# Kernel optimization log

Hardware: AMD Instinct MI355X
Metric: run time of the kernel (lower is better)

Reference implementation:

```python
import jax, jax.numpy as jnp
import numpy as np
from jax import lax

EPS = 1e-5
B, C, H, W = 16, 256, 56, 56
HEADS, DIM_K, DIM_U, DIM_OUT = 4, 16, 4, 256
DIM_V = DIM_OUT // HEADS  # 64
R = 15


def setup_inputs() -> dict:
    key = jax.random.key(0)
    ks = jax.random.split(key, 16)
    s = 0.05
    return {
        "x": jax.random.normal(ks[0], (B, C, H, W), jnp.float32),
        "Wq": jax.random.normal(ks[1], (C, HEADS * DIM_K), jnp.float32) * s,
        "Wk": jax.random.normal(ks[2], (C, DIM_U * DIM_K), jnp.float32) * s,
        "Wv": jax.random.normal(ks[3], (C, DIM_U * DIM_V), jnp.float32) * s,
        "pos_w": jax.random.normal(ks[4], (DIM_K, DIM_U, 1, R, R), jnp.float32) * s,
        "pos_b": jax.random.normal(ks[5], (DIM_K,), jnp.float32) * s,
        "gq": jax.random.uniform(ks[6], (HEADS * DIM_K,), jnp.float32),
        "bq": jax.random.normal(ks[7], (HEADS * DIM_K,), jnp.float32) * s,
        "mq": jax.random.normal(ks[8], (HEADS * DIM_K,), jnp.float32) * s,
        "vq": jax.random.uniform(ks[9], (HEADS * DIM_K,), jnp.float32) + 0.5,
        "gv": jax.random.uniform(ks[10], (DIM_U * DIM_V,), jnp.float32),
        "bv": jax.random.normal(ks[11], (DIM_U * DIM_V,), jnp.float32) * s,
        "mv": jax.random.normal(ks[12], (DIM_U * DIM_V,), jnp.float32) * s,
        "vv": jax.random.uniform(ks[13], (DIM_U * DIM_V,), jnp.float32) + 0.5,
    }


def _bn(x, gamma, beta, mean, var):
    # inference-mode BatchNorm over channel dim (axis=1), x: [b,c,h,w]
    inv = gamma / jnp.sqrt(var + EPS)
    return x * inv[None, :, None, None] + (beta - mean * inv)[None, :, None, None]


def reference(x, Wq, Wk, Wv, pos_w, pos_b, gq, bq, mq, vq, gv, bv, mv, vv):
    b, c, hh, ww = x.shape
    n = hh * ww
    h, dk, u, dv = HEADS, DIM_K, DIM_U, DIM_V
    # 1x1 convs (channels_first) == channel matmuls
    q = jnp.einsum('bchw,cd->bdhw', x, Wq)
    k = jnp.einsum('bchw,cd->bdhw', x, Wk)
    v = jnp.einsum('bchw,cd->bdhw', x, Wv)
    q = _bn(q, gq, bq, mq, vq)
    v = _bn(v, gv, bv, mv, vv)
    # rearranges: 'b (h k) hh ww -> b h k (hh ww)', 'b (u k) hh ww -> b u k n', 'b (u v) hh ww -> b u v n'
    q = q.reshape(b, h, dk, n)
    k = k.reshape(b, u, dk, n)
    v = v.reshape(b, u, dv, n)
    k = jax.nn.softmax(k, axis=-1)  # keras Softmax default axis=-1 (positions)
    # content lambda
    Lc = jnp.einsum('bukm,buvm->bkv', k, v)
    Yc = jnp.einsum('bhkn,bkv->bnhv', q, Lc)
    # position lambda: conv3d over (v,hh,ww) with kernel (1,r,r), pad spatial only
    v5 = v.reshape(b, u, dv, hh, ww)  # [N, C=u, D=v, H, W]
    p = R // 2
    Lp = lax.conv_general_dilated(
        v5, pos_w, window_strides=(1, 1, 1),
        padding=[(0, 0), (p, p), (p, p)],
        dimension_numbers=('NCDHW', 'OIDHW', 'NCDHW'))
    Lp = Lp + pos_b[None, :, None, None, None]  # [b, k, v, hh, ww]
    Lp = Lp.reshape(b, dk, dv, n)
    Yp = jnp.einsum('bhkn,bkvn->bnhv', q, Lp)
    Y = Yc + Yp  # [b, n, h, v]
    # 'b (hh ww) h v -> b (h v) hh ww'
    out = Y.reshape(b, hh, ww, h, dv).transpose(0, 3, 4, 1, 2).reshape(b, h * dv, hh, ww)
    return out
```

## Files before the change

kernel.cpp:

```cpp
#include <hip/hip_runtime.h>
#include <cstdint>
#include <cstddef>

#define NB   16
#define NC   256
#define NPIX 3136
#define NW   56
#define EPSV 1e-5f

#define OFF_AB   0u
#define OFF_BNA  49152u
#define OFF_BNB  49536u
#define OFF_WT   49920u
#define OFF_KS   58112u
#define OFF_LC   59136u
#define OFF_Y    75520u

typedef short bf16x8 __attribute__((ext_vector_type(8)));
typedef float f32x4  __attribute__((ext_vector_type(4)));
typedef float f32x16 __attribute__((ext_vector_type(16)));

__device__ __forceinline__ uint32_t f2bf(float f) {
  uint32_t x = __float_as_uint(f);
  uint32_t r = x + 0x7fffu + ((x >> 16) & 1u);
  return r >> 16;
}

__device__ __forceinline__ float fetchW(const float* Wq, const float* Wk,
                                        const float* Wv, int m, int c) {
  if (m < 64)  return Wq[c * 64 + m];
  if (m < 128) return Wk[c * 64 + (m - 64)];
  return Wv[c * 256 + (m - 128)];
}

__global__ void prep_kernel(const float* __restrict__ Wq, const float* __restrict__ Wk,
                            const float* __restrict__ Wv, const float* __restrict__ pos_w,
                            const float* __restrict__ gq, const float* __restrict__ bq,
                            const float* __restrict__ mq, const float* __restrict__ vq,
                            const float* __restrict__ gv, const float* __restrict__ bv,
                            const float* __restrict__ mv, const float* __restrict__ vv,
                            float* __restrict__ ws) {
  int d = blockIdx.x;
  int c = threadIdx.x;
  int i = d * 256 + c;
  if (i < 49152) {
    int dgt = i >> 12, rem = i & 4095;
    int kc = rem >> 8, rem2 = rem & 255;
    int lane = rem2 >> 2, dp = rem2 & 3;
    int m = dgt * 32 + (lane & 31);
    int k0 = kc * 16 + (lane >> 5) * 8 + dp * 2;
    float w0 = fetchW(Wq, Wk, Wv, m, k0);
    float w1 = fetchW(Wq, Wk, Wv, m, k0 + 1);
    ((uint32_t*)(ws + OFF_AB))[i] = f2bf(w0) | (f2bf(w1) << 16);
  }
  if (c == 0) {
    float sa, sb;
    if (d < 64)        { float inv = gq[d] / sqrtf(vq[d] + EPSV); sa = inv; sb = bq[d] - mq[d] * inv; }
    else if (d < 128)  { sa = 1.0f; sb = 0.0f; }
    else               { int j = d - 128; float inv = gv[j] / sqrtf(vv[j] + EPSV); sa = inv; sb = bv[j] - mv[j] * inv; }
    ws[OFF_BNA + d] = sa;
    ws[OFF_BNB + d] = sb;
  }
  if (i < 8192) {
    int chunk = i >> 8, rem = i & 255, lane = rem >> 2, dp = rem & 3;
    int quad = lane >> 4, k = lane & 15;
    int u = chunk >> 3, t = chunk & 7;
    int dh = 2 * t + (quad >> 1);
    int dwb = (quad & 1) * 8 + dp * 2;
    float w0 = (dh < 15 && dwb     < 15) ? pos_w[k * 900 + u * 225 + dh * 15 + dwb]     : 0.0f;
    float w1 = (dh < 15 && dwb + 1 < 15) ? pos_w[k * 900 + u * 225 + dh * 15 + dwb + 1] : 0.0f;
    ((uint32_t*)(ws + OFF_WT))[i] = f2bf(w0) | (f2bf(w1) << 16);
  }
  if (i < 1024) ws[OFF_KS + i] = 0.0f;
}

__launch_bounds__(256, 2)
__global__ void qkv_mfma(const float* __restrict__ x, const float* __restrict__ wsc,
                         float* __restrict__ Y) {
  __shared__ uint32_t X[64 * 128];
  __shared__ float BNs[768];
  int tid = threadIdx.x;
  int n0 = blockIdx.x * 64, b = blockIdx.y;
  for (int i = tid; i < 768; i += 256) BNs[i] = wsc[OFF_BNA + i];
  const size_t xb = (size_t)b * NC * NPIX;
#pragma unroll
  for (int it = 0; it < 4; ++it) {
    int n2 = tid & 31;
    int cp4 = it * 8 + (tid >> 5);
    const float* xp = x + xb + (size_t)(cp4 * 8) * NPIX + n0 + n2 * 2;
    float2 ld[8];
#pragma unroll
    for (int j = 0; j < 8; ++j) ld[j] = *(const float2*)(xp + (size_t)j * NPIX);
    uint32_t e0, e1, e2, e3, o0, o1, o2, o3;
    e0 = f2bf(ld[0].x) | (f2bf(ld[1].x) << 16);
    e1 = f2bf(ld[2].x) | (f2bf(ld[3].x) << 16);
    e2 = f2bf(ld[4].x) | (f2bf(ld[5].x) << 16);
    e3 = f2bf(ld[6].x) | (f2bf(ld[7].x) << 16);
    o0 = f2bf(ld[0].y) | (f2bf(ld[1].y) << 16);
    o1 = f2bf(ld[2].y) | (f2bf(ld[3].y) << 16);
    o2 = f2bf(ld[4].y) | (f2bf(ld[5].y) << 16);
    o3 = f2bf(ld[6].y) | (f2bf(ld[7].y) << 16);
    int ne = 2 * n2, no = ne + 1;
    uint4 ve; ve.x = e0; ve.y = e1; ve.z = e2; ve.w = e3;
    uint4 vo; vo.x = o0; vo.y = o1; vo.z = o2; vo.w = o3;
    *(uint4*)(X + ne * 128 + ((cp4 ^ (ne & 31)) << 2)) = ve;
    *(uint4*)(X + no * 128 + ((cp4 ^ (no & 31)) << 2)) = vo;
  }
  __syncthreads();
  int lane = tid & 63, w = tid >> 6;
  int n31 = lane & 31, h5 = lane >> 5;
  f32x16 acc[3][2];
#pragma unroll
  for (int dt = 0; dt < 3; ++dt)
#pragma unroll
    for (int nt = 0; nt < 2; ++nt)
#pragma unroll
      for (int e = 0; e < 16; ++e) acc[dt][nt][e] = 0.0f;
  const uint4* AB = (const uint4*)(wsc + OFF_AB);
#pragma unroll 4
  for (int kc = 0; kc < 16; ++kc) {
    bf16x8 af[3];
#pragma unroll
    for (int dt = 0; dt < 3; ++dt) {
      union { uint4 q; bf16x8 v; } tmp;
      tmp.q = AB[(size_t)(((w * 3 + dt) * 16 + kc)) * 64 + lane];
      af[dt] = tmp.v;
    }
#pragma unroll
    for (int nt = 0; nt < 2; ++nt) {
      union { uint4 q; bf16x8 v; } bu;
      bu.q = *(const uint4*)(X + (nt * 32 + n31) * 128 + (((2 * kc + h5) ^ n31) << 2));
#pragma unroll
      for (int dt = 0; dt < 3; ++dt)
        acc[dt][nt] = __builtin_amdgcn_mfma_f32_32x32x16_bf16(af[dt], bu.v, acc[dt][nt], 0, 0, 0);
    }
  }
#pragma unroll
  for (int dt = 0; dt < 3; ++dt) {
    int dgt = w * 3 + dt;
    float sa[16], sb[16];
#pragma unroll
    for (int g = 0; g < 4; ++g) {
      *(float4*)(sa + g * 4) = *(const float4*)(BNs + dgt * 32 + g * 8 + h5 * 4);
      *(float4*)(sb + g * 4) = *(const float4*)(BNs + 384 + dgt * 32 + g * 8 + h5 * 4);
    }
#pragma unroll
    for (int nt = 0; nt < 2; ++nt) {
      int pix = n0 + nt * 32 + n31;
      if (dgt < 2) {
        uint2* qb2 = (uint2*)(Y + (size_t)b * 384 * NPIX);
#pragma unroll
        for (int g = 0; g < 4; ++g) {
          float y0 = fmaf(acc[dt][nt][4 * g + 0], sa[4 * g + 0], sb[4 * g + 0]);
          float y1 = fmaf(acc[dt][nt][4 * g + 1], sa[4 * g + 1], sb[4 * g + 1]);
          float y2 = fmaf(acc[dt][nt][4 * g + 2], sa[4 * g + 2], sb[4 * g + 2]);
          float y3 = fmaf(acc[dt][nt][4 * g + 3], sa[4 * g + 3], sb[4 * g + 3]);
          uint2 val;
          val.x = f2bf(y0) | (f2bf(y1) << 16);
          val.y = f2bf(y2) | (f2bf(y3) << 16);
          qb2[(size_t)(dgt * 8 + 2 * g + h5) * NPIX + pix] = val;
        }
      } else {
#pragma unroll
        for (int g = 0; g < 4; ++g)
#pragma unroll
          for (int ki = 0; ki < 4; ++ki) {
            int d = dgt * 32 + 8 * g + 4 * h5 + ki;
            Y[((size_t)b * 384 + d) * NPIX + pix] =
                fmaf(acc[dt][nt][4 * g + ki], sa[4 * g + ki], sb[4 * g + ki]);
          }
      }
    }
  }
}

__launch_bounds__(256)
__global__ void lc_mfma(float* __restrict__ Y, float* __restrict__ ws) {
  int ks = blockIdx.x, u = blockIdx.y, b = blockIdx.z;
  int tid = threadIdx.x;
  int lane = tid & 63, w = tid >> 6;
  int col = lane & 15, quad = lane >> 4;
  int slot = ks * 4 + w;
  const float* krow  = Y + ((size_t)(b * 384 + 64 + u * 16 + col)) * NPIX;
  const float* vbase = Y + ((size_t)(b * 384 + 128 + u * 64 + col)) * NPIX;
  f32x4 acc[4];
#pragma unroll
  for (int vt = 0; vt < 4; ++vt) acc[vt] = (f32x4){0.f, 0.f, 0.f, 0.f};
  float ssum = 0.0f;
  for (int c = slot; c < 98; c += 16) {
    int n0 = c * 32 + quad * 8;
    float4 k0 = *(const float4*)(krow + n0);
    float4 k1 = *(const float4*)(krow + n0 + 4);
    float e0 = __expf(k0.x), e1 = __expf(k0.y), e2 = __expf(k0.z), e3 = __expf(k0.w);
    float e4 = __expf(k1.x), e5 = __expf(k1.y), e6 = __expf(k1.z), e7 = __expf(k1.w);
    ssum += (e0 + e1 + e2 + e3) + (e4 + e5 + e6 + e7);
    union { uint32_t d[4]; bf16x8 v; } kb;
    kb.d[0] = f2bf(e0) | (f2bf(e1) << 16);
    kb.d[1] = f2bf(e2) | (f2bf(e3) << 16);
    kb.d[2] = f2bf(e4) | (f2bf(e5) << 16);
    kb.d[3] = f2bf(e6) | (f2bf(e7) << 16);
#pragma unroll
    for (int vt = 0; vt < 4; ++vt) {
      const float* vp = vbase + (size_t)(vt * 16) * NPIX + n0;
      float4 v0 = *(const float4*)(vp);
      float4 v1 = *(const float4*)(vp + 4);
      union { uint32_t d[4]; bf16x8 v; } vb;
      vb.d[0] = f2bf(v0.x) | (f2bf(v0.y) << 16);
      vb.d[1] = f2bf(v0.z) | (f2bf(v0.w) << 16);
      vb.d[2] = f2bf(v1.x) | (f2bf(v1.y) << 16);
      vb.d[3] = f2bf(v1.z) | (f2bf(v1.w) << 16);
      acc[vt] = __builtin_amdgcn_mfma_f32_16x16x32_bf16(vb.v, kb.v, acc[vt], 0, 0, 0);
    }
  }
  ssum += __shfl_xor(ssum, 16);
  ssum += __shfl_xor(ssum, 32);
  if (lane < 16) atomicAdd(&ws[OFF_KS + b * 64 + u * 16 + col], ssum);
  float* P = Y + (size_t)b * 384 * NPIX + 32 * NPIX + (size_t)(u * 16 + slot) * 1024;
#pragma unroll
  for (int vt = 0; vt < 4; ++vt)
#pragma unroll
    for (int r = 0; r < 4; ++r)
      P[vt * 256 + quad * 64 + r * 16 + col] = acc[vt][r];
}

__global__ void lc_reduce(const float* __restrict__ Y, float* __restrict__ ws) {
  int i = blockIdx.x, b = blockIdx.y;
  int t = threadIdx.x;
  __shared__ float invS[64];
  if (t < 64) invS[t] = 1.0f / ws[OFF_KS + b * 64 + t];
  __syncthreads();
  int idx = i * 256 + t;
  int k = idx & 15, v = idx >> 4;
  const float* P = Y + (size_t)b * 384 * NPIX + 32 * NPIX;
  float tot = 0.0f;
#pragma unroll
  for (int u = 0; u < 4; ++u) {
    float su = 0.0f;
#pragma unroll
    for (int s = 0; s < 16; ++s) su += P[(size_t)(u * 16 + s) * 1024 + idx];
    tot += su * invS[u * 16 + k];
  }
  ws[OFF_LC + (b * 16 + k) * 64 + v] = tot;
}

#define ROWS   29
#define RSTR2  74
#define UPITCH2 2146
#define LDSW2  8584

__launch_bounds__(512, 4)
__global__ void pos_lambda_mfma(const float* __restrict__ Y, const float* __restrict__ wsc,
                                const float* __restrict__ pos_b, float* __restrict__ out) {
  __shared__ uint32_t S[LDSW2];
  int v = blockIdx.x, b = blockIdx.y, band = blockIdx.z;
  int rb = band * 14;
  int tid = threadIdx.x;
  for (int i = tid; i < LDSW2; i += 512) {
    int u = i / UPITCH2; int rem = i - u * UPITCH2;
    int prow = rem / RSTR2; int pos = rem - prow * RSTR2;
    int gr = rb + prow - 7;
    float f0 = 0.0f, f1 = 0.0f;
    if (gr >= 0 && gr < NW && pos < 72) {
      const float* vp = Y + ((size_t)(b * 384 + 128 + u * 64 + v)) * NPIX + gr * NW;
      int g0 = pos - 7, g1 = pos - 6;
      if (g0 >= 0 && g0 < NW) f0 = vp[g0];
      if (g1 >= 0 && g1 < NW) f1 = vp[g1];
    }
    S[i] = f2bf(f0) | (f2bf(f1) << 16);
  }
  __syncthreads();
  int lane = tid & 63, wid = tid >> 6;
  int quad = lane >> 4, n = lane & 15;
  int dhp = quad >> 1;
  int ct = wid & 3, p = wid >> 2;
  int cb = (ct == 3) ? 40 : ct * 16;
  int sb = cb + n + (quad & 1) * 8;
  int abase = (p + dhp) * RSTR2 + sb;
  const uint4* wt = (const uint4*)(wsc + OFF_WT);
  f32x4 acc[7];
#pragma unroll
  for (int q = 0; q < 7; ++q) acc[q] = (f32x4){0.f, 0.f, 0.f, 0.f};
#pragma unroll 1
  for (int u = 0; u < 4; ++u) {
    bf16x8 wf[8];
#pragma unroll
    for (int t = 0; t < 8; ++t) {
      union { uint4 q; bf16x8 v; } tmp;
      tmp.q = wt[(u * 8 + t) * 64 + lane];
      wf[t] = tmp.v;
    }
    int au = u * UPITCH2 + abase;
#pragma unroll
    for (int PP = 0; PP < 14; ++PP) {
      int a = au + PP * (2 * RSTR2);
      union { uint32_t u4[4]; bf16x8 v8; } bu;
      bu.u4[0] = S[a];     bu.u4[1] = S[a + 2];
      bu.u4[2] = S[a + 4]; bu.u4[3] = S[a + 6];
#pragma unroll
      for (int t = 0; t < 8; ++t) {
        int q = PP - t;
        if (q >= 0 && q < 7)
          acc[q] = __builtin_amdgcn_mfma_f32_16x16x32_bf16(wf[t], bu.v8, acc[q], 0, 0, 0);
      }
    }
  }
  float lcq[4];
#pragma unroll
  for (int r = 0; r < 4; ++r) {
    int k = quad * 4 + r;
    lcq[r] = wsc[OFF_LC + (b * 16 + k) * 64 + v] + pos_b[k];
  }
  const uint2* qb2 = (const uint2*)(Y + (size_t)b * 384 * NPIX);
#pragma unroll
  for (int q = 0; q < 7; ++q) {
    int rr = rb + p + 2 * q;
    int pix = rr * NW + cb + n;
    float m0 = acc[q][0] + lcq[0], m1 = acc[q][1] + lcq[1];
    float m2 = acc[q][2] + lcq[2], m3 = acc[q][3] + lcq[3];
    float pp[4];
#pragma unroll
    for (int j = 0; j < 4; ++j) {
      int h = quad ^ j;
      uint2 qd = qb2[(h * 4 + quad) * NPIX + pix];
      float q0 = __uint_as_float(qd.x << 16);
      float q1 = __uint_as_float(qd.x & 0xffff0000u);
      float q2 = __uint_as_float(qd.y << 16);
      float q3 = __uint_as_float(qd.y & 0xffff0000u);
      pp[j] = fmaf(q0, m0, fmaf(q1, m1, fmaf(q2, m2, q3 * m3)));
    }
    float t0 = pp[0] + __shfl_xor(pp[1], 16);
    float t2 = pp[2] + __shfl_xor(pp[3], 16);
    float y  = t0 + __shfl_xor(t2, 32);
    out[((size_t)(b * 256 + quad * 64 + v)) * NPIX + pix] = y;
  }
}

extern "C" void kernel_launch(void* const* d_in, const int* in_sizes, int n_in,
                              void* d_out, int out_size, void* d_ws, size_t ws_size,
                              hipStream_t stream) {
  const float* x     = (const float*)d_in[0];
  const float* Wq    = (const float*)d_in[1];
  const float* Wk    = (const float*)d_in[2];
  const float* Wv    = (const float*)d_in[3];
  const float* pos_w = (const float*)d_in[4];
  const float* pos_b = (const float*)d_in[5];
  const float* gq    = (const float*)d_in[6];
  const float* bq    = (const float*)d_in[7];
  const float* mq    = (const float*)d_in[8];
  const float* vq    = (const float*)d_in[9];
  const float* gv    = (const float*)d_in[10];
  const float* bv    = (const float*)d_in[11];
  const float* mv    = (const float*)d_in[12];
  const float* vv    = (const float*)d_in[13];
  float* ws  = (float*)d_ws;
  float* out = (float*)d_out;
  float* Y   = ws + OFF_Y;

  prep_kernel<<<dim3(384), 256, 0, stream>>>(Wq, Wk, Wv, pos_w, gq, bq, mq, vq,
                                             gv, bv, mv, vv, ws);
  qkv_mfma<<<dim3(49, 16), 256, 0, stream>>>(x, ws, Y);
  lc_mfma<<<dim3(4, 4, 16), 256, 0, stream>>>(Y, ws);
  lc_reduce<<<dim3(4, 16), 256, 0, stream>>>(Y, ws);
  pos_lambda_mfma<<<dim3(64, 16, 4), 512, 0, stream>>>(Y, ws, pos_b, out);
}
```

Measured before the change: 274.9 us.

## Widen lc_mfma grid with LDS partial reduction; vectorize pos-lambda staging with truncating bf16 pack

```diff
diff --git a/kernel.cpp b/kernel.cpp
--- a/kernel.cpp
+++ b/kernel.cpp
@@ -24,6 +24,9 @@
   uint32_t x = __float_as_uint(f);
   uint32_t r = x + 0x7fffu + ((x >> 16) & 1u);
   return r >> 16;
+}
+__device__ __forceinline__ uint32_t pk_trunc(float a, float b) {
+  return (__float_as_uint(a) >> 16) | (__float_as_uint(b) & 0xffff0000u);
 }
 
 __device__ __forceinline__ float fetchW(const float* Wq, const float* Wk,
@@ -176,18 +179,20 @@
 
 __launch_bounds__(256)
 __global__ void lc_mfma(float* __restrict__ Y, float* __restrict__ ws) {
-  int ks = blockIdx.x, u = blockIdx.y, b = blockIdx.z;
+  __shared__ float R[4096];
+  __shared__ float Rs[64];
+  int bx = blockIdx.x, u = blockIdx.y, b = blockIdx.z;
   int tid = threadIdx.x;
   int lane = tid & 63, w = tid >> 6;
   int col = lane & 15, quad = lane >> 4;
-  int slot = ks * 4 + w;
+  int slot = bx * 4 + w;
   const float* krow  = Y + ((size_t)(b * 384 + 64 + u * 16 + col)) * NPIX;
   const float* vbase = Y + ((size_t)(b * 384 + 128 + u * 64 + col)) * NPIX;
   f32x4 acc[4];
 #pragma unroll
   for (int vt = 0; vt < 4; ++vt) acc[vt] = (f32x4){0.f, 0.f, 0.f, 0.f};
   float ssum = 0.0f;
-  for (int c = slot; c < 98; c += 16) {
+  for (int c = slot; c < 98; c += 64) {
     int n0 = c * 32 + quad * 8;
     float4 k0 = *(const float4*)(krow + n0);
     float4 k1 = *(const float4*)(krow + n0 + 4);
@@ -195,32 +200,46 @@
     float e4 = __expf(k1.x), e5 = __expf(k1.y), e6 = __expf(k1.z), e7 = __expf(k1.w);
     ssum += (e0 + e1 + e2 + e3) + (e4 + e5 + e6 + e7);
     union { uint32_t d[4]; bf16x8 v; } kb;
-    kb.d[0] = f2bf(e0) | (f2bf(e1) << 16);
-    kb.d[1] = f2bf(e2) | (f2bf(e3) << 16);
-    kb.d[2] = f2bf(e4) | (f2bf(e5) << 16);
-    kb.d[3] = f2bf(e6) | (f2bf(e7) << 16);
+    kb.d[0] = pk_trunc(e0, e1);
+    kb.d[1] = pk_trunc(e2, e3);
+    kb.d[2] = pk_trunc(e4, e5);
+    kb.d[3] = pk_trunc(e6, e7);
 #pragma unroll
     for (int vt = 0; vt < 4; ++vt) {
       const float* vp = vbase + (size_t)(vt * 16) * NPIX + n0;
       float4 v0 = *(const float4*)(vp);
       float4 v1 = *(const float4*)(vp + 4);
       union { uint32_t d[4]; bf16x8 v; } vb;
-      vb.d[0] = f2bf(v0.x) | (f2bf(v0.y) << 16);
-      vb.d[1] = f2bf(v0.z) | (f2bf(v0.w) << 16);
-      vb.d[2] = f2bf(v1.x) | (f2bf(v1.y) << 16);
-      vb.d[3] = f2bf(v1.z) | (f2bf(v1.w) << 16);
+      vb.d[0] = pk_trunc(v0.x, v0.y);
+      vb.d[1] = pk_trunc(v0.z, v0.w);
+      vb.d[2] = pk_trunc(v1.x, v1.y);
+      vb.d[3] = pk_trunc(v1.z, v1.w);
       acc[vt] = __builtin_amdgcn_mfma_f32_16x16x32_bf16(vb.v, kb.v, acc[vt], 0, 0, 0);
     }
   }
   ssum += __shfl_xor(ssum, 16);
   ssum += __shfl_xor(ssum, 32);
-  if (lane < 16) atomicAdd(&ws[OFF_KS + b * 64 + u * 16 + col], ssum);
-  float* P = Y + (size_t)b * 384 * NPIX + 32 * NPIX + (size_t)(u * 16 + slot) * 1024;
 #pragma unroll
   for (int vt = 0; vt < 4; ++vt)
 #pragma unroll
     for (int r = 0; r < 4; ++r)
-      P[vt * 256 + quad * 64 + r * 16 + col] = acc[vt][r];
+      R[w * 1024 + vt * 256 + quad * 64 + r * 16 + col] = acc[vt][r];
+  if (lane < 16) Rs[w * 16 + col] = ssum;
+  __syncthreads();
+  float* P = Y + (size_t)b * 384 * NPIX + 32 * NPIX + (size_t)(u * 16 + bx) * 1024;
+  float4 s0 = *(const float4*)(R + tid * 4);
+  float4 s1 = *(const float4*)(R + 1024 + tid * 4);
+  float4 s2 = *(const float4*)(R + 2048 + tid * 4);
+  float4 s3 = *(const float4*)(R + 3072 + tid * 4);
+  float4 tot;
+  tot.x = (s0.x + s1.x) + (s2.x + s3.x);
+  tot.y = (s0.y + s1.y) + (s2.y + s3.y);
+  tot.z = (s0.z + s1.z) + (s2.z + s3.z);
+  tot.w = (s0.w + s1.w) + (s2.w + s3.w);
+  *(float4*)(P + tid * 4) = tot;
+  if (tid < 16)
+    atomicAdd(&ws[OFF_KS + b * 64 + u * 16 + tid],
+              (Rs[tid] + Rs[16 + tid]) + (Rs[32 + tid] + Rs[48 + tid]));
 }
 
 __global__ void lc_reduce(const float* __restrict__ Y, float* __restrict__ ws) {
@@ -255,18 +274,29 @@
   int v = blockIdx.x, b = blockIdx.y, band = blockIdx.z;
   int rb = band * 14;
   int tid = threadIdx.x;
-  for (int i = tid; i < LDSW2; i += 512) {
-    int u = i / UPITCH2; int rem = i - u * UPITCH2;
-    int prow = rem / RSTR2; int pos = rem - prow * RSTR2;
-    int gr = rb + prow - 7;
-    float f0 = 0.0f, f1 = 0.0f;
-    if (gr >= 0 && gr < NW && pos < 72) {
-      const float* vp = Y + ((size_t)(b * 384 + 128 + u * 64 + v)) * NPIX + gr * NW;
-      int g0 = pos - 7, g1 = pos - 6;
-      if (g0 >= 0 && g0 < NW) f0 = vp[g0];
-      if (g1 >= 0 && g1 < NW) f1 = vp[g1];
-    }
-    S[i] = f2bf(f0) | (f2bf(f1) << 16);
+  const float* vplane = Y + ((size_t)(b * 384 + 128)) * NPIX + v * NPIX;
+  for (int ii = tid; ii < 4292; ii += 512) {
+    int u = ii / 1073;
+    int rem = ii - u * 1073;
+    int row = rem / 37;
+    int pr = rem - row * 37;
+    int gr = rb + row - 7;
+    int grc = min(max(gr, 0), NW - 1);
+    bool rv = (gr >= 0) && (gr < NW);
+    const float* vp = vplane + (size_t)(u * 64) * NPIX + grc * NW;
+    int g0 = 2 * pr - 7;
+    float e[3];
+#pragma unroll
+    for (int j = 0; j < 3; ++j) {
+      int g = g0 + j;
+      int gc = min(max(g, 0), NW - 1);
+      float val = vp[gc];
+      e[j] = (rv && g >= 0 && g < NW) ? val : 0.0f;
+    }
+    uint2 dd;
+    dd.x = pk_trunc(e[0], e[1]);
+    dd.y = pk_trunc(e[1], e[2]);
+    *(uint2*)(S + u * UPITCH2 + row * RSTR2 + 2 * pr) = dd;
   }
   __syncthreads();
   int lane = tid & 63, wid = tid >> 6;
@@ -359,7 +389,7 @@
   prep_kernel<<<dim3(384), 256, 0, stream>>>(Wq, Wk, Wv, pos_w, gq, bq, mq, vq,
                                              gv, bv, mv, vv, ws);
   qkv_mfma<<<dim3(49, 16), 256, 0, stream>>>(x, ws, Y);
-  lc_mfma<<<dim3(4, 4, 16), 256, 0, stream>>>(Y, ws);
+  lc_mfma<<<dim3(16, 4, 16), 256, 0, stream>>>(Y, ws);
   lc_reduce<<<dim3(4, 16), 256, 0, stream>>>(Y, ws);
   pos_lambda_mfma<<<dim3(64, 16, 4), 512, 0, stream>>>(Y, ws, pos_b, out);
 }
```

Measured after the change: 269.6 us. No clear change (-1.9%).
